# Performance work log

Hardware: AMD Instinct MI355X
Metric: run time of the kernel (lower is better)

Reference implementation:

```python
import jax, jax.numpy as jnp
import numpy as np

LN_EPS = 1e-5


def setup_inputs() -> dict:
    key = jax.random.key(0)
    k1, k2, k3 = jax.random.split(key, 3)
    B, C, N, T, K = 8, 64, 512, 288, 32
    x = jax.random.normal(k1, (B, C, N, T), dtype=jnp.float32)
    HEs = jax.random.uniform(k2, (N, K), dtype=jnp.float32)  # relu(tanh(...)) in [0,1)
    edge_map = jax.random.normal(k3, (K, K), dtype=jnp.float32) / np.sqrt(K)
    return {"x": x, "HEs": HEs, "edge_map": edge_map}


def reference(x, HEs, edge_map):
    # x: [B, C, N, T]; HEs: [N, K]; edge_map: [K, K]
    B, C, N, T = x.shape
    xt = jnp.transpose(x, (0, 3, 2, 1))            # [B, T, N, C]
    feat = xt.reshape(B * T, N, C)                 # [B*T, N, C]
    # hyperedge aggregation: HEs^T @ feat
    hyper_feat = jnp.einsum('nk,bnc->bkc', HEs, feat)          # [B*T, K, C]
    hyper_mapped = jax.nn.relu(jnp.einsum('kj,bjc->bkc', edge_map, hyper_feat))
    hyper_out = hyper_mapped + hyper_feat
    # scatter back to nodes
    y = jax.nn.relu(jnp.einsum('nk,bkc->bnc', HEs, hyper_out)) # [B*T, N, C]
    y = y.reshape(B, T, N, C)
    z = y + xt
    # fresh LayerNorm over last dim (C), affine params are identity (ones/zeros)
    mu = jnp.mean(z, axis=-1, keepdims=True)
    var = jnp.mean(jnp.square(z - mu), axis=-1, keepdims=True)
    z = (z - mu) * jax.lax.rsqrt(var + LN_EPS)
    return jnp.transpose(z, (0, 3, 2, 1))          # [B, C, N, T]
```

## Files before the change

### kernel.cpp

```cpp
#include <hip/hip_runtime.h>

#define B_ 8
#define C_ 64
#define N_ 512
#define T_ 288
#define K_ 32

typedef __bf16 bf16;
typedef __attribute__((ext_vector_type(4))) __bf16 bf16x4;
typedef __attribute__((ext_vector_type(8))) __bf16 bf16x8;
typedef __attribute__((ext_vector_type(4))) float f32x4;

__device__ __forceinline__ float ldin(const void* p, int f32, size_t i) {
    if (f32) return ((const float*)p)[i];
    return (float)((const bf16*)p)[i];
}

__global__ void k_detect(const void* __restrict__ x, int* __restrict__ flag) {
    __shared__ float sm[256];
    const bf16* xb = (const bf16*)x;
    float m = 0.f;
    for (int i = threadIdx.x; i < 4096; i += 256) {
        float a = fabsf((float)xb[i]);
        if (!(a <= 1000.f)) a = 1e30f;
        m = fmaxf(m, a);
    }
    sm[threadIdx.x] = m;
    __syncthreads();
    if (threadIdx.x == 0) {
        float mm = 0.f;
        for (int i = 0; i < 256; ++i) mm = fmaxf(mm, sm[i]);
        *flag = (mm > 1000.f) ? 1 : 0;
    }
}

__global__ void k_prep(const void* __restrict__ hes, const void* __restrict__ em,
                       const int* __restrict__ flag,
                       bf16* __restrict__ hesb, bf16* __restrict__ hest,
                       bf16* __restrict__ emb) {
    const int f32 = *flag;
    int idx = blockIdx.x * 256 + threadIdx.x;
    if (idx < N_ * K_) {
        float v = ldin(hes, f32, idx);
        hesb[idx] = (bf16)v;
        int n = idx >> 5, k = idx & 31;
        hest[k * N_ + n] = (bf16)v;
    }
    if (idx < K_ * K_) emb[idx] = (bf16)ldin(em, f32, idx);
}

__global__ __launch_bounds__(64) void k_hyper(const void* __restrict__ x,
                                              const int* __restrict__ flag,
                                              const bf16* __restrict__ hest,
                                              const bf16* __restrict__ emb,
                                              bf16* __restrict__ ho) {
    const int f32 = *flag;
    const int tile = blockIdx.x, c = blockIdx.y, b = blockIdx.z;
    const int lane = threadIdx.x;
    const int col  = lane & 15;
    const int q    = lane >> 4;
    const int t0   = tile * 32;
    const size_t xbase = ((size_t)(b * C_ + c)) * N_ * T_;

    f32x4 acc[2][2] = {};
    for (int step = 0; step < 16; ++step) {
        const int nb = step * 32;
        bf16x8 a0 = *(const bf16x8*)(hest + (size_t)(col) * N_ + nb + 8 * q);
        bf16x8 a1 = *(const bf16x8*)(hest + (size_t)(16 + col) * N_ + nb + 8 * q);
        bf16x8 b0, b1;
        const size_t xq = xbase + (size_t)(nb + 8 * q) * T_ + t0;
        #pragma unroll
        for (int j = 0; j < 8; ++j) {
            b0[j] = (bf16)ldin(x, f32, xq + (size_t)j * T_ + col);
            b1[j] = (bf16)ldin(x, f32, xq + (size_t)j * T_ + 16 + col);
        }
        acc[0][0] = __builtin_amdgcn_mfma_f32_16x16x32_bf16(a0, b0, acc[0][0], 0, 0, 0);
        acc[0][1] = __builtin_amdgcn_mfma_f32_16x16x32_bf16(a0, b1, acc[0][1], 0, 0, 0);
        acc[1][0] = __builtin_amdgcn_mfma_f32_16x16x32_bf16(a1, b0, acc[1][0], 0, 0, 0);
        acc[1][1] = __builtin_amdgcn_mfma_f32_16x16x32_bf16(a1, b1, acc[1][1], 0, 0, 0);
    }

    __shared__ float hf[K_][33];
    #pragma unroll
    for (int mt = 0; mt < 2; ++mt)
        #pragma unroll
        for (int tt = 0; tt < 2; ++tt)
            #pragma unroll
            for (int r = 0; r < 4; ++r)
                hf[16 * mt + 4 * q + r][16 * tt + col] = acc[mt][tt][r];
    __syncthreads();

    f32x4 acc2[2][2];
    #pragma unroll
    for (int mt = 0; mt < 2; ++mt) {
        bf16x8 a = *(const bf16x8*)(emb + (size_t)(16 * mt + col) * K_ + 8 * q);
        #pragma unroll
        for (int tt = 0; tt < 2; ++tt) {
            bf16x8 bb;
            #pragma unroll
            for (int jj = 0; jj < 8; ++jj)
                bb[jj] = (bf16)hf[8 * q + jj][16 * tt + col];
            f32x4 zero = {};
            acc2[mt][tt] = __builtin_amdgcn_mfma_f32_16x16x32_bf16(a, bb, zero, 0, 0, 0);
        }
    }

    #pragma unroll
    for (int mt = 0; mt < 2; ++mt)
        #pragma unroll
        for (int tt = 0; tt < 2; ++tt) {
            bf16x4 v;
            #pragma unroll
            for (int r = 0; r < 4; ++r) {
                float hv = acc2[mt][tt][r];
                hv = hv > 0.f ? hv : 0.f;
                hv += acc[mt][tt][r];
                v[r] = (bf16)hv;
            }
            *(bf16x4*)(ho + (((size_t)(b * C_ + c)) * T_ + t0 + 16 * tt + col) * K_
                          + 16 * mt + 4 * q) = v;
        }
}

__global__ __launch_bounds__(256) void k_scatter_ln(const void* __restrict__ x,
                                                    const int* __restrict__ flag,
                                                    const bf16* __restrict__ hesb,
                                                    const bf16* __restrict__ ho,
                                                    void* __restrict__ outp) {
    const int f32 = *flag;
    const int t0 = blockIdx.x * 16;
    const int n0 = blockIdx.y * 16;
    const int b  = blockIdx.z;
    const int tid  = threadIdx.x;
    const int w    = tid >> 6;
    const int lane = tid & 63;
    const int col  = lane & 15;
    const int q    = lane >> 4;

    bf16x8 a = *(const bf16x8*)(hesb + (size_t)(n0 + col) * K_ + 8 * q);

    f32x4 z[16];
    const bf16* hob = ho + (((size_t)(b * C_)) * T_ + t0 + col) * K_ + 8 * q;
    #pragma unroll
    for (int i = 0; i < 16; ++i) {
        int c = w * 16 + i;
        bf16x8 bb = *(const bf16x8*)(hob + (size_t)c * T_ * K_);
        f32x4 zero = {};
        z[i] = __builtin_amdgcn_mfma_f32_16x16x32_bf16(a, bb, zero, 0, 0, 0);
    }

    float s1[4] = {0.f, 0.f, 0.f, 0.f}, s2[4] = {0.f, 0.f, 0.f, 0.f};
    const size_t xb = ((size_t)b * C_) * (size_t)N_ * T_;
    #pragma unroll
    for (int i = 0; i < 16; ++i) {
        int c = w * 16 + i;
        #pragma unroll
        for (int r = 0; r < 4; ++r) {
            int row = q * 4 + r;
            float zz = z[i][r];
            zz = zz > 0.f ? zz : 0.f;
            zz += ldin(x, f32, xb + ((size_t)c * N_ + n0 + row) * T_ + t0 + col);
            z[i][r] = zz;
            s1[r] += zz;
            s2[r] += zz * zz;
        }
    }

    __shared__ float sh1[4][16][17];
    __shared__ float sh2[4][16][17];
    #pragma unroll
    for (int r = 0; r < 4; ++r) {
        sh1[w][q * 4 + r][col] = s1[r];
        sh2[w][q * 4 + r][col] = s2[r];
    }
    __syncthreads();

    {
        int rr = tid >> 4, cc = tid & 15;
        float S1 = sh1[0][rr][cc] + sh1[1][rr][cc] + sh1[2][rr][cc] + sh1[3][rr][cc];
        float S2 = sh2[0][rr][cc] + sh2[1][rr][cc] + sh2[2][rr][cc] + sh2[3][rr][cc];
        float mu  = S1 * (1.f / 64.f);
        float var = S2 * (1.f / 64.f) - mu * mu;
        float rs  = rsqrtf(var + 1e-5f);
        sh1[0][rr][cc] = mu;
        sh2[0][rr][cc] = rs;
    }
    __syncthreads();

    float mu_r[4], rs_r[4];
    #pragma unroll
    for (int r = 0; r < 4; ++r) {
        mu_r[r] = sh1[0][q * 4 + r][col];
        rs_r[r] = sh2[0][q * 4 + r][col];
    }
    #pragma unroll
    for (int i = 0; i < 16; ++i) {
        int c = w * 16 + i;
        size_t ob = ((size_t)(b * C_ + c) * N_ + n0) * T_ + t0 + col;
        #pragma unroll
        for (int r = 0; r < 4; ++r) {
            float v = (z[i][r] - mu_r[r]) * rs_r[r];
            size_t idx = ob + (size_t)(q * 4 + r) * T_;
            if (f32) ((float*)outp)[idx] = v;
            else     ((bf16*)outp)[idx] = (bf16)v;
        }
    }
}

extern "C" void kernel_launch(void* const* d_in, const int* in_sizes, int n_in,
                              void* d_out, int out_size, void* d_ws, size_t ws_size,
                              hipStream_t stream) {
    const void* x   = d_in[0];
    const void* hes = d_in[1];
    const void* em  = d_in[2];

    char* ws = (char*)d_ws;
    int*  flag = (int*)ws;
    bf16* hesb = (bf16*)(ws + 64);
    bf16* hest = hesb + (size_t)N_ * K_;
    bf16* emb  = hest + (size_t)K_ * N_;
    bf16* ho   = emb  + (size_t)K_ * K_;

    k_detect<<<1, 256, 0, stream>>>(x, flag);
    k_prep<<<dim3((N_ * K_ + 255) / 256), 256, 0, stream>>>(hes, em, flag, hesb, hest, emb);
    k_hyper<<<dim3(T_ / 32, C_, B_), 64, 0, stream>>>(x, flag, hest, emb, ho);
    k_scatter_ln<<<dim3(T_ / 16, N_ / 16, B_), 256, 0, stream>>>(x, flag, hesb, ho, d_out);
}
```

Before: 702.6 us.

## Stage x through LDS, vectorize global loads/stores, merge detect into prep

The dtype-detection kernel is merged into the prep kernel, and each block now computes the flag itself with a tree reduction. The hyper kernel stages 128-row chunks of x into shared memory with vectorized coalesced loads and transposes them for the MFMA B operand. The scatter/LayerNorm kernel now swaps MFMA operands so each lane holds 4 consecutive T values, which allows vectorized x loads and output stores. It also uses 512-thread blocks covering 32 timesteps and a flat grid with batch interleaving. Both kernels template on the dtype flag to remove per-element branches. The cost is extra LDS use and syncs in the hyper kernel.

```diff
diff --git a/kernel.cpp b/kernel.cpp
--- a/kernel.cpp
+++ b/kernel.cpp
@@ -11,12 +11,13 @@
 typedef __attribute__((ext_vector_type(8))) __bf16 bf16x8;
 typedef __attribute__((ext_vector_type(4))) float f32x4;
 
-__device__ __forceinline__ float ldin(const void* p, int f32, size_t i) {
-    if (f32) return ((const float*)p)[i];
-    return (float)((const bf16*)p)[i];
-}
-
-__global__ void k_detect(const void* __restrict__ x, int* __restrict__ flag) {
+__global__ __launch_bounds__(256) void k_prep(const void* __restrict__ x,
+                                              const void* __restrict__ hes,
+                                              const void* __restrict__ em,
+                                              bf16* __restrict__ hesb,
+                                              bf16* __restrict__ hest,
+                                              bf16* __restrict__ emb,
+                                              int* __restrict__ flag) {
     __shared__ float sm[256];
     const bf16* xb = (const bf16*)x;
     float m = 0.f;
@@ -27,34 +28,31 @@
     }
     sm[threadIdx.x] = m;
     __syncthreads();
-    if (threadIdx.x == 0) {
-        float mm = 0.f;
-        for (int i = 0; i < 256; ++i) mm = fmaxf(mm, sm[i]);
-        *flag = (mm > 1000.f) ? 1 : 0;
-    }
-}
-
-__global__ void k_prep(const void* __restrict__ hes, const void* __restrict__ em,
-                       const int* __restrict__ flag,
-                       bf16* __restrict__ hesb, bf16* __restrict__ hest,
-                       bf16* __restrict__ emb) {
-    const int f32 = *flag;
+    for (int s = 128; s > 0; s >>= 1) {
+        if (threadIdx.x < s) sm[threadIdx.x] = fmaxf(sm[threadIdx.x], sm[threadIdx.x + s]);
+        __syncthreads();
+    }
+    const int f32 = (sm[0] > 1000.f) ? 1 : 0;
+    if (blockIdx.x == 0 && threadIdx.x == 0) *flag = f32;
+
     int idx = blockIdx.x * 256 + threadIdx.x;
     if (idx < N_ * K_) {
-        float v = ldin(hes, f32, idx);
+        float v = f32 ? ((const float*)hes)[idx] : (float)((const bf16*)hes)[idx];
         hesb[idx] = (bf16)v;
         int n = idx >> 5, k = idx & 31;
         hest[k * N_ + n] = (bf16)v;
     }
-    if (idx < K_ * K_) emb[idx] = (bf16)ldin(em, f32, idx);
-}
-
-__global__ __launch_bounds__(64) void k_hyper(const void* __restrict__ x,
-                                              const int* __restrict__ flag,
-                                              const bf16* __restrict__ hest,
-                                              const bf16* __restrict__ emb,
-                                              bf16* __restrict__ ho) {
-    const int f32 = *flag;
+    if (idx < K_ * K_) {
+        float v = f32 ? ((const float*)em)[idx] : (float)((const bf16*)em)[idx];
+        emb[idx] = (bf16)v;
+    }
+}
+
+template <int F32>
+__device__ __forceinline__ void hyper_body(const void* __restrict__ x,
+                                           const bf16* __restrict__ hest,
+                                           const bf16* __restrict__ emb,
+                                           bf16* __restrict__ ho) {
     const int tile = blockIdx.x, c = blockIdx.y, b = blockIdx.z;
     const int lane = threadIdx.x;
     const int col  = lane & 15;
@@ -62,25 +60,49 @@
     const int t0   = tile * 32;
     const size_t xbase = ((size_t)(b * C_ + c)) * N_ * T_;
 
+    __shared__ bf16  xT[32][136];
+    __shared__ float hf[K_][33];
+
+    const int tq = lane & 7;
+    const int rw = lane >> 3;
+
     f32x4 acc[2][2] = {};
-    for (int step = 0; step < 16; ++step) {
-        const int nb = step * 32;
-        bf16x8 a0 = *(const bf16x8*)(hest + (size_t)(col) * N_ + nb + 8 * q);
-        bf16x8 a1 = *(const bf16x8*)(hest + (size_t)(16 + col) * N_ + nb + 8 * q);
-        bf16x8 b0, b1;
-        const size_t xq = xbase + (size_t)(nb + 8 * q) * T_ + t0;
-        #pragma unroll
-        for (int j = 0; j < 8; ++j) {
-            b0[j] = (bf16)ldin(x, f32, xq + (size_t)j * T_ + col);
-            b1[j] = (bf16)ldin(x, f32, xq + (size_t)j * T_ + 16 + col);
-        }
-        acc[0][0] = __builtin_amdgcn_mfma_f32_16x16x32_bf16(a0, b0, acc[0][0], 0, 0, 0);
-        acc[0][1] = __builtin_amdgcn_mfma_f32_16x16x32_bf16(a0, b1, acc[0][1], 0, 0, 0);
-        acc[1][0] = __builtin_amdgcn_mfma_f32_16x16x32_bf16(a1, b0, acc[1][0], 0, 0, 0);
-        acc[1][1] = __builtin_amdgcn_mfma_f32_16x16x32_bf16(a1, b1, acc[1][1], 0, 0, 0);
-    }
-
-    __shared__ float hf[K_][33];
+    for (int chunk = 0; chunk < 4; ++chunk) {
+        const int nc = chunk * 128;
+        #pragma unroll
+        for (int it = 0; it < 16; ++it) {
+            const int row = it * 8 + rw;
+            const size_t gi = xbase + (size_t)(nc + row) * T_ + t0 + 4 * tq;
+            float v0, v1, v2, v3;
+            if (F32) {
+                f32x4 v = *(const f32x4*)((const float*)x + gi);
+                v0 = v[0]; v1 = v[1]; v2 = v[2]; v3 = v[3];
+            } else {
+                bf16x4 v = *(const bf16x4*)((const bf16*)x + gi);
+                v0 = (float)v[0]; v1 = (float)v[1]; v2 = (float)v[2]; v3 = (float)v[3];
+            }
+            xT[4 * tq + 0][row] = (bf16)v0;
+            xT[4 * tq + 1][row] = (bf16)v1;
+            xT[4 * tq + 2][row] = (bf16)v2;
+            xT[4 * tq + 3][row] = (bf16)v3;
+        }
+        __syncthreads();
+        #pragma unroll
+        for (int s = 0; s < 4; ++s) {
+            const int nl = s * 32;
+            const int ng = nc + nl;
+            bf16x8 a0 = *(const bf16x8*)(hest + (size_t)(col) * N_ + ng + 8 * q);
+            bf16x8 a1 = *(const bf16x8*)(hest + (size_t)(16 + col) * N_ + ng + 8 * q);
+            bf16x8 b0 = *(const bf16x8*)(&xT[col][nl + 8 * q]);
+            bf16x8 b1 = *(const bf16x8*)(&xT[16 + col][nl + 8 * q]);
+            acc[0][0] = __builtin_amdgcn_mfma_f32_16x16x32_bf16(a0, b0, acc[0][0], 0, 0, 0);
+            acc[0][1] = __builtin_amdgcn_mfma_f32_16x16x32_bf16(a0, b1, acc[0][1], 0, 0, 0);
+            acc[1][0] = __builtin_amdgcn_mfma_f32_16x16x32_bf16(a1, b0, acc[1][0], 0, 0, 0);
+            acc[1][1] = __builtin_amdgcn_mfma_f32_16x16x32_bf16(a1, b1, acc[1][1], 0, 0, 0);
+        }
+        __syncthreads();
+    }
+
     #pragma unroll
     for (int mt = 0; mt < 2; ++mt)
         #pragma unroll
@@ -122,89 +144,122 @@
         }
 }
 
-__global__ __launch_bounds__(256) void k_scatter_ln(const void* __restrict__ x,
-                                                    const int* __restrict__ flag,
-                                                    const bf16* __restrict__ hesb,
-                                                    const bf16* __restrict__ ho,
-                                                    void* __restrict__ outp) {
-    const int f32 = *flag;
-    const int t0 = blockIdx.x * 16;
-    const int n0 = blockIdx.y * 16;
-    const int b  = blockIdx.z;
-    const int tid  = threadIdx.x;
-    const int w    = tid >> 6;
-    const int lane = tid & 63;
-    const int col  = lane & 15;
-    const int q    = lane >> 4;
-
-    bf16x8 a = *(const bf16x8*)(hesb + (size_t)(n0 + col) * K_ + 8 * q);
+__global__ __launch_bounds__(64, 3) void k_hyper(const void* __restrict__ x,
+                                                 const int* __restrict__ flag,
+                                                 const bf16* __restrict__ hest,
+                                                 const bf16* __restrict__ emb,
+                                                 bf16* __restrict__ ho) {
+    if (*flag) hyper_body<1>(x, hest, emb, ho);
+    else       hyper_body<0>(x, hest, emb, ho);
+}
+
+template <int F32>
+__device__ __forceinline__ void scatter_body(const void* __restrict__ x,
+                                             const bf16* __restrict__ hesb,
+                                             const bf16* __restrict__ ho,
+                                             void* __restrict__ outp) {
+    const int wg  = blockIdx.x;
+    const int b   = wg & 7;
+    const int pos = wg >> 3;
+    const int bx  = pos % 9;
+    const int n0  = (pos / 9) * 16;
+
+    const int tid   = threadIdx.x;
+    const int w     = tid >> 6;
+    const int lane  = tid & 63;
+    const int col   = lane & 15;
+    const int q     = lane >> 4;
+    const int thalf = w & 1;
+    const int cgrp  = w >> 1;
+    const int t0    = bx * 32 + thalf * 16;
+
+    bf16x8 hb = *(const bf16x8*)(hesb + (size_t)(n0 + col) * K_ + 8 * q);
 
     f32x4 z[16];
+    float s1[4] = {0.f, 0.f, 0.f, 0.f}, s2[4] = {0.f, 0.f, 0.f, 0.f};
     const bf16* hob = ho + (((size_t)(b * C_)) * T_ + t0 + col) * K_ + 8 * q;
+    const size_t xb = ((size_t)b * C_) * (size_t)N_ * T_;
     #pragma unroll
     for (int i = 0; i < 16; ++i) {
-        int c = w * 16 + i;
-        bf16x8 bb = *(const bf16x8*)(hob + (size_t)c * T_ * K_);
+        const int c = cgrp * 16 + i;
+        bf16x8 a = *(const bf16x8*)(hob + (size_t)c * T_ * K_);
         f32x4 zero = {};
-        z[i] = __builtin_amdgcn_mfma_f32_16x16x32_bf16(a, bb, zero, 0, 0, 0);
-    }
-
-    float s1[4] = {0.f, 0.f, 0.f, 0.f}, s2[4] = {0.f, 0.f, 0.f, 0.f};
-    const size_t xb = ((size_t)b * C_) * (size_t)N_ * T_;
-    #pragma unroll
-    for (int i = 0; i < 16; ++i) {
-        int c = w * 16 + i;
+        f32x4 zz = __builtin_amdgcn_mfma_f32_16x16x32_bf16(a, hb, zero, 0, 0, 0);
+        const size_t xi = xb + ((size_t)c * N_ + n0 + col) * T_ + t0 + 4 * q;
+        f32x4 xv;
+        if (F32) {
+            xv = *(const f32x4*)((const float*)x + xi);
+        } else {
+            bf16x4 x4 = *(const bf16x4*)((const bf16*)x + xi);
+            xv[0] = (float)x4[0]; xv[1] = (float)x4[1];
+            xv[2] = (float)x4[2]; xv[3] = (float)x4[3];
+        }
         #pragma unroll
         for (int r = 0; r < 4; ++r) {
-            int row = q * 4 + r;
-            float zz = z[i][r];
-            zz = zz > 0.f ? zz : 0.f;
-            zz += ldin(x, f32, xb + ((size_t)c * N_ + n0 + row) * T_ + t0 + col);
-            z[i][r] = zz;
-            s1[r] += zz;
-            s2[r] += zz * zz;
-        }
-    }
-
-    __shared__ float sh1[4][16][17];
-    __shared__ float sh2[4][16][17];
+            float v = zz[r];
+            v = v > 0.f ? v : 0.f;
+            v += xv[r];
+            zz[r] = v;
+            s1[r] += v;
+            s2[r] += v * v;
+        }
+        z[i] = zz;
+    }
+
+    __shared__ float sh1[2][4][16][17];
+    __shared__ float sh2[2][4][16][17];
     #pragma unroll
     for (int r = 0; r < 4; ++r) {
-        sh1[w][q * 4 + r][col] = s1[r];
-        sh2[w][q * 4 + r][col] = s2[r];
+        sh1[thalf][cgrp][4 * q + r][col] = s1[r];
+        sh2[thalf][cgrp][4 * q + r][col] = s2[r];
     }
     __syncthreads();
 
     {
-        int rr = tid >> 4, cc = tid & 15;
-        float S1 = sh1[0][rr][cc] + sh1[1][rr][cc] + sh1[2][rr][cc] + sh1[3][rr][cc];
-        float S2 = sh2[0][rr][cc] + sh2[1][rr][cc] + sh2[2][rr][cc] + sh2[3][rr][cc];
+        const int th = tid >> 8, rr = (tid >> 4) & 15, cc = tid & 15;
+        float S1 = sh1[th][0][rr][cc] + sh1[th][1][rr][cc]
+                 + sh1[th][2][rr][cc] + sh1[th][3][rr][cc];
+        float S2 = sh2[th][0][rr][cc] + sh2[th][1][rr][cc]
+                 + sh2[th][2][rr][cc] + sh2[th][3][rr][cc];
         float mu  = S1 * (1.f / 64.f);
         float var = S2 * (1.f / 64.f) - mu * mu;
         float rs  = rsqrtf(var + 1e-5f);
-        sh1[0][rr][cc] = mu;
-        sh2[0][rr][cc] = rs;
+        sh1[th][0][rr][cc] = mu;
+        sh2[th][0][rr][cc] = rs;
     }
     __syncthreads();
 
     float mu_r[4], rs_r[4];
     #pragma unroll
     for (int r = 0; r < 4; ++r) {
-        mu_r[r] = sh1[0][q * 4 + r][col];
-        rs_r[r] = sh2[0][q * 4 + r][col];
+        mu_r[r] = sh1[thalf][0][4 * q + r][col];
+        rs_r[r] = sh2[thalf][0][4 * q + r][col];
     }
     #pragma unroll
     for (int i = 0; i < 16; ++i) {
-        int c = w * 16 + i;
-        size_t ob = ((size_t)(b * C_ + c) * N_ + n0) * T_ + t0 + col;
-        #pragma unroll
-        for (int r = 0; r < 4; ++r) {
-            float v = (z[i][r] - mu_r[r]) * rs_r[r];
-            size_t idx = ob + (size_t)(q * 4 + r) * T_;
-            if (f32) ((float*)outp)[idx] = v;
-            else     ((bf16*)outp)[idx] = (bf16)v;
-        }
-    }
+        const int c = cgrp * 16 + i;
+        const size_t oi = ((size_t)(b * C_ + c) * N_ + n0 + col) * T_ + t0 + 4 * q;
+        if (F32) {
+            f32x4 v;
+            #pragma unroll
+            for (int r = 0; r < 4; ++r) v[r] = (z[i][r] - mu_r[r]) * rs_r[r];
+            *(f32x4*)((float*)outp + oi) = v;
+        } else {
+            bf16x4 v;
+            #pragma unroll
+            for (int r = 0; r < 4; ++r) v[r] = (bf16)((z[i][r] - mu_r[r]) * rs_r[r]);
+            *(bf16x4*)((bf16*)outp + oi) = v;
+        }
+    }
+}
+
+__global__ __launch_bounds__(512, 2) void k_scatter_ln(const void* __restrict__ x,
+                                                       const int* __restrict__ flag,
+                                                       const bf16* __restrict__ hesb,
+                                                       const bf16* __restrict__ ho,
+                                                       void* __restrict__ outp) {
+    if (*flag) scatter_body<1>(x, hesb, ho, outp);
+    else       scatter_body<0>(x, hesb, ho, outp);
 }
 
 extern "C" void kernel_launch(void* const* d_in, const int* in_sizes, int n_in,
@@ -221,8 +276,7 @@
     bf16* emb  = hest + (size_t)K_ * N_;
     bf16* ho   = emb  + (size_t)K_ * K_;
 
-    k_detect<<<1, 256, 0, stream>>>(x, flag);
-    k_prep<<<dim3((N_ * K_ + 255) / 256), 256, 0, stream>>>(hes, em, flag, hesb, hest, emb);
+    k_prep<<<dim3((N_ * K_ + 255) / 256), 256, 0, stream>>>(x, hes, em, hesb, hest, emb, flag);
     k_hyper<<<dim3(T_ / 32, C_, B_), 64, 0, stream>>>(x, flag, hest, emb, ho);
-    k_scatter_ln<<<dim3(T_ / 16, N_ / 16, B_), 256, 0, stream>>>(x, flag, hesb, ho, d_out);
-}
+    k_scatter_ln<<<dim3((T_ / 32) * (N_ / 16) * B_, 1, 1), 512, 0, stream>>>(x, flag, hesb, ho, d_out);
+}
```

New measurement: 603.1 us. 14.2% less time.
